# Kernel tuning notes

Measured on AMD Instinct MI355X. Metric: run time of the kernel, lower is better.

Reference implementation:

```python
import jax, jax.numpy as jnp
import numpy as np

B, N, L = 64, 256, 1024
OUT = L // 2   # ChebConv out_channels = Seq_len / 2
ALPHA = 0.5    # DirGNNConv default alpha


def _glorot(key, shape):
    # PyG ChebConv lins use glorot init
    lim = float(np.sqrt(6.0 / (shape[0] + shape[1])))
    return jax.random.uniform(key, shape, minval=-lim, maxval=lim, dtype=jnp.float32)


def setup_inputs() -> dict:
    key = jax.random.key(0)
    ks = jax.random.split(key, 8)
    x = jax.random.normal(ks[0], (B, N, L), dtype=jnp.float32)
    # dense per-sample adjacency; only used via nonzero() in torch, never enters math (K=1)
    At = jax.random.randint(ks[1], (B, N, N), 0, 2, dtype=jnp.int32)
    W_in = _glorot(ks[2], (L, OUT))
    b_in = jnp.zeros((OUT,), dtype=jnp.float32)
    W_out = _glorot(ks[3], (L, OUT))
    b_out = jnp.zeros((OUT,), dtype=jnp.float32)
    # DirGNNConv root Linear (kaiming-ish uniform; exact init irrelevant for correctness baseline)
    lim = float(1.0 / np.sqrt(L))
    W_root = jax.random.uniform(ks[4], (L, OUT), minval=-lim, maxval=lim, dtype=jnp.float32)
    b_root = jax.random.uniform(ks[5], (OUT,), minval=-lim, maxval=lim, dtype=jnp.float32)
    return {"x": x, "At": At, "W_in": W_in, "b_in": b_in,
            "W_out": W_out, "b_out": b_out, "W_root": W_root, "b_root": b_root}


def reference(x, At, W_in, b_in, W_out, b_out, W_root, b_root):
    # so the batched edge_index built from At.nonzero() never influences the output.
    # DirGNNConv: alpha * conv_out(x) + (1-alpha) * conv_in(x) + root_lin(x).
    xf = x.reshape(B * N, L)                        # [B*N, L]
    y = (ALPHA * (xf @ W_out + b_out)
         + (1.0 - ALPHA) * (xf @ W_in + b_in)
         + (xf @ W_root + b_root))                  # [B*N, OUT]
    return y.reshape(B, N, OUT)
```

## Files before the change

kernel.cpp:

```cpp
#include <hip/hip_runtime.h>
#include <stdint.h>

static constexpr int Mrows = 16384;
static constexpr int Kdim  = 1024;
static constexpr int Ncols = 512;

typedef __attribute__((ext_vector_type(8))) short bf16x8;
typedef __attribute__((ext_vector_type(4))) float f32x4;

__device__ __forceinline__ unsigned short f2bf(float f) {
  unsigned u = __builtin_bit_cast(unsigned, f);
  u += 0x7FFFu + ((u >> 16) & 1u);
  return (unsigned short)(u >> 16);
}
__device__ __forceinline__ unsigned f2bf2(float lo, float hi) {
  unsigned ul = __builtin_bit_cast(unsigned, lo);
  unsigned uh = __builtin_bit_cast(unsigned, hi);
  ul += 0x7FFFu + ((ul >> 16) & 1u);
  uh += 0x7FFFu + ((uh >> 16) & 1u);
  return (ul >> 16) | (uh & 0xFFFF0000u);
}

__global__ __launch_bounds__(256) void combine_w(
    const float* __restrict__ Win, const float* __restrict__ Wout,
    const float* __restrict__ Wroot, unsigned short* __restrict__ Wt)
{
  __shared__ unsigned short lds[32 * 36];
  const int bid = blockIdx.x;
  const int tk0 = (bid & 31) * 32;
  const int tn0 = (bid >> 5) * 32;
  const int t = threadIdx.x;
  {
    const int k  = t >> 3;
    const int nq = (t & 7) * 4;
    const int gi = (tk0 + k) * Ncols + tn0 + nq;
    const float4 wi = *(const float4*)(Win + gi);
    const float4 wo = *(const float4*)(Wout + gi);
    const float4 wr = *(const float4*)(Wroot + gi);
    lds[(nq + 0) * 36 + k] = f2bf(0.5f * (wi.x + wo.x) + wr.x);
    lds[(nq + 1) * 36 + k] = f2bf(0.5f * (wi.y + wo.y) + wr.y);
    lds[(nq + 2) * 36 + k] = f2bf(0.5f * (wi.z + wo.z) + wr.z);
    lds[(nq + 3) * 36 + k] = f2bf(0.5f * (wi.w + wo.w) + wr.w);
  }
  __syncthreads();
  {
    const int n  = t >> 3;
    const int k8 = (t & 7) * 4;
    const ushort4 v = *(const ushort4*)&lds[n * 36 + k8];
    *(ushort4*)(Wt + (size_t)(tn0 + n) * Kdim + tk0 + k8) = v;
  }
}

__global__ __launch_bounds__(256) void gemm_fused(
    const float* __restrict__ X, const unsigned short* __restrict__ Wt,
    const float* __restrict__ b_in, const float* __restrict__ b_out,
    const float* __restrict__ b_root, float* __restrict__ Y)
{
  __shared__ short Asl[128 * 40];
  __shared__ short Bsl[128 * 40];

  const int bid = blockIdx.x;
  const int m0 = (bid & 127) * 128;
  const int n0 = (bid >> 7) * 128;

  const int t    = threadIdx.x;
  const int lane = t & 63;
  const int wid  = t >> 6;
  const int wm   = wid >> 1;
  const int wn   = wid & 1;
  const int quad = lane >> 4;
  const int lm   = lane & 15;

  const int sr = t >> 1;
  const int sh = t & 1;
  const float*          xp = X  + (size_t)(m0 + sr) * Kdim + sh * 16;
  const unsigned short* wp = Wt + (size_t)(n0 + sr) * Kdim + sh * 16;
  const int sbase = sr * 40 + sh * 16;

  f32x4 acc[4][4] = {};

  float4 a0 = *(const float4*)(xp + 0);
  float4 a1 = *(const float4*)(xp + 4);
  float4 a2 = *(const float4*)(xp + 8);
  float4 a3 = *(const float4*)(xp + 12);
  uint4  bA = *(const uint4*)(wp);
  uint4  bB = *(const uint4*)(wp + 8);

  const int arow0 = (wm * 64 + lm) * 40 + quad * 8;
  const int brow0 = (wn * 64 + lm) * 40 + quad * 8;

  #pragma unroll 1
  for (int it = 0; it < 32; ++it) {
    __syncthreads();
    uint4 p0, p1;
    p0.x = f2bf2(a0.x, a0.y); p0.y = f2bf2(a0.z, a0.w);
    p0.z = f2bf2(a1.x, a1.y); p0.w = f2bf2(a1.z, a1.w);
    p1.x = f2bf2(a2.x, a2.y); p1.y = f2bf2(a2.z, a2.w);
    p1.z = f2bf2(a3.x, a3.y); p1.w = f2bf2(a3.z, a3.w);
    *(uint4*)&Asl[sbase]     = p0;
    *(uint4*)&Asl[sbase + 8] = p1;
    *(uint4*)&Bsl[sbase]     = bA;
    *(uint4*)&Bsl[sbase + 8] = bB;
    __syncthreads();

    if (it < 31) {
      const float* xn = xp + (it + 1) * 32;
      a0 = *(const float4*)(xn + 0);
      a1 = *(const float4*)(xn + 4);
      a2 = *(const float4*)(xn + 8);
      a3 = *(const float4*)(xn + 12);
      const unsigned short* wn2 = wp + (it + 1) * 32;
      bA = *(const uint4*)(wn2);
      bB = *(const uint4*)(wn2 + 8);
    }

    bf16x8 af[4], bfr[4];
    #pragma unroll
    for (int i = 0; i < 4; ++i) af[i]  = *(const bf16x8*)&Asl[arow0 + i * 16 * 40];
    #pragma unroll
    for (int j = 0; j < 4; ++j) bfr[j] = *(const bf16x8*)&Bsl[brow0 + j * 16 * 40];

    #pragma unroll
    for (int i = 0; i < 4; ++i)
      #pragma unroll
      for (int j = 0; j < 4; ++j)
        acc[i][j] = __builtin_amdgcn_mfma_f32_16x16x32_bf16(af[i], bfr[j], acc[i][j], 0, 0, 0);
  }

  #pragma unroll
  for (int j = 0; j < 4; ++j) {
    const int gc = n0 + wn * 64 + j * 16 + lm;
    const float bias = 0.5f * (b_in[gc] + b_out[gc]) + b_root[gc];
    #pragma unroll
    for (int i = 0; i < 4; ++i) {
      const int gr = m0 + wm * 64 + i * 16 + quad * 4;
      float* yp = Y + (size_t)gr * Ncols + gc;
      #pragma unroll
      for (int r = 0; r < 4; ++r)
        yp[(size_t)r * Ncols] = acc[i][j][r] + bias;
    }
  }
}

extern "C" void kernel_launch(void* const* d_in, const int* in_sizes, int n_in,
                              void* d_out, int out_size, void* d_ws, size_t ws_size,
                              hipStream_t stream)
{
  const float* x      = (const float*)d_in[0];
  const float* W_in   = (const float*)d_in[2];
  const float* b_in   = (const float*)d_in[3];
  const float* W_out  = (const float*)d_in[4];
  const float* b_out  = (const float*)d_in[5];
  const float* W_root = (const float*)d_in[6];
  const float* b_root = (const float*)d_in[7];
  float* y = (float*)d_out;

  unsigned short* Wt = (unsigned short*)d_ws;

  combine_w<<<dim3(512), dim3(256), 0, stream>>>(W_in, W_out, W_root, Wt);
  gemm_fused<<<dim3(512), dim3(256), 0, stream>>>(x, Wt, b_in, b_out, b_root, y);
}
```

Measured before the change: 155.7 us.

## Pre-convert X to bf16 and stage GEMM tiles via direct global-to-LDS loads

Adds a prep pass that converts X to bf16 into workspace, merged into one launch with the weight-combine blocks. The GEMM then streams bf16 tiles with global_load_lds into an XOR-swizzled unpadded LDS layout and drops the register prefetch and in-loop conversion. This cuts in-loop ALU work and register pressure, and launch bounds now request two blocks per SM. The cost is an extra full read and write of X through HBM, plus less overlap, since each iteration waits on its own loads before the MFMAs.

```diff
diff --git a/kernel.cpp b/kernel.cpp
--- a/kernel.cpp
+++ b/kernel.cpp
@@ -21,43 +21,62 @@
   return (ul >> 16) | (uh & 0xFFFF0000u);
 }
 
-__global__ __launch_bounds__(256) void combine_w(
+__device__ __forceinline__ void gl2lds16(const void* g, void* l) {
+  __builtin_amdgcn_global_load_lds(
+      (const __attribute__((address_space(1))) void*)g,
+      (__attribute__((address_space(3))) void*)l, 16, 0, 0);
+}
+
+__global__ __launch_bounds__(256) void prep(
+    const float* __restrict__ x,
     const float* __restrict__ Win, const float* __restrict__ Wout,
-    const float* __restrict__ Wroot, unsigned short* __restrict__ Wt)
+    const float* __restrict__ Wroot,
+    unsigned short* __restrict__ Xbf, unsigned short* __restrict__ Wt)
 {
-  __shared__ unsigned short lds[32 * 36];
   const int bid = blockIdx.x;
-  const int tk0 = (bid & 31) * 32;
-  const int tn0 = (bid >> 5) * 32;
   const int t = threadIdx.x;
-  {
-    const int k  = t >> 3;
-    const int nq = (t & 7) * 4;
-    const int gi = (tk0 + k) * Ncols + tn0 + nq;
-    const float4 wi = *(const float4*)(Win + gi);
-    const float4 wo = *(const float4*)(Wout + gi);
-    const float4 wr = *(const float4*)(Wroot + gi);
-    lds[(nq + 0) * 36 + k] = f2bf(0.5f * (wi.x + wo.x) + wr.x);
-    lds[(nq + 1) * 36 + k] = f2bf(0.5f * (wi.y + wo.y) + wr.y);
-    lds[(nq + 2) * 36 + k] = f2bf(0.5f * (wi.z + wo.z) + wr.z);
-    lds[(nq + 3) * 36 + k] = f2bf(0.5f * (wi.w + wo.w) + wr.w);
-  }
-  __syncthreads();
-  {
-    const int n  = t >> 3;
-    const int k8 = (t & 7) * 4;
-    const ushort4 v = *(const ushort4*)&lds[n * 36 + k8];
-    *(ushort4*)(Wt + (size_t)(tn0 + n) * Kdim + tk0 + k8) = v;
+  if (bid < 8192) {
+    const size_t base = ((size_t)bid * 256 + t) * 8;
+    const float4 v0 = *(const float4*)(x + base);
+    const float4 v1 = *(const float4*)(x + base + 4);
+    uint4 p;
+    p.x = f2bf2(v0.x, v0.y); p.y = f2bf2(v0.z, v0.w);
+    p.z = f2bf2(v1.x, v1.y); p.w = f2bf2(v1.z, v1.w);
+    *(uint4*)(Xbf + base) = p;
+  } else {
+    __shared__ unsigned short lds[32 * 36];
+    const int b2 = bid - 8192;
+    const int tk0 = (b2 & 31) * 32;
+    const int tn0 = (b2 >> 5) * 32;
+    {
+      const int k  = t >> 3;
+      const int nq = (t & 7) * 4;
+      const int gi = (tk0 + k) * Ncols + tn0 + nq;
+      const float4 wi = *(const float4*)(Win + gi);
+      const float4 wo = *(const float4*)(Wout + gi);
+      const float4 wr = *(const float4*)(Wroot + gi);
+      lds[(nq + 0) * 36 + k] = f2bf(0.5f * (wi.x + wo.x) + wr.x);
+      lds[(nq + 1) * 36 + k] = f2bf(0.5f * (wi.y + wo.y) + wr.y);
+      lds[(nq + 2) * 36 + k] = f2bf(0.5f * (wi.z + wo.z) + wr.z);
+      lds[(nq + 3) * 36 + k] = f2bf(0.5f * (wi.w + wo.w) + wr.w);
+    }
+    __syncthreads();
+    {
+      const int n  = t >> 3;
+      const int k8 = (t & 7) * 4;
+      const ushort4 v = *(const ushort4*)&lds[n * 36 + k8];
+      *(ushort4*)(Wt + (size_t)(tn0 + n) * Kdim + tk0 + k8) = v;
+    }
   }
 }
 
-__global__ __launch_bounds__(256) void gemm_fused(
-    const float* __restrict__ X, const unsigned short* __restrict__ Wt,
+__global__ __launch_bounds__(256, 2) void gemm_bf16(
+    const unsigned short* __restrict__ Xbf, const unsigned short* __restrict__ Wt,
     const float* __restrict__ b_in, const float* __restrict__ b_out,
     const float* __restrict__ b_root, float* __restrict__ Y)
 {
-  __shared__ short Asl[128 * 40];
-  __shared__ short Bsl[128 * 40];
+  __shared__ __attribute__((aligned(16))) short As[128 * 32];
+  __shared__ __attribute__((aligned(16))) short Bs[128 * 32];
 
   const int bid = blockIdx.x;
   const int m0 = (bid & 127) * 128;
@@ -65,66 +84,52 @@
 
   const int t    = threadIdx.x;
   const int lane = t & 63;
-  const int wid  = t >> 6;
-  const int wm   = wid >> 1;
-  const int wn   = wid & 1;
+  const int w    = t >> 6;
+  const int wm   = w >> 1;
+  const int wn   = w & 1;
   const int quad = lane >> 4;
   const int lm   = lane & 15;
 
-  const int sr = t >> 1;
-  const int sh = t & 1;
-  const float*          xp = X  + (size_t)(m0 + sr) * Kdim + sh * 16;
-  const unsigned short* wp = Wt + (size_t)(n0 + sr) * Kdim + sh * 16;
-  const int sbase = sr * 40 + sh * 16;
+  const int sr = lane >> 2;
+  const int ss = lane & 3;
+  const int sc = ss ^ ((sr >> 1) & 3);
+  const unsigned short* gA = Xbf + (size_t)(m0 + w * 32 + sr) * Kdim + sc * 8;
+  const unsigned short* gB = Wt  + (size_t)(n0 + w * 32 + sr) * Kdim + sc * 8;
+  short* const lA0 = &As[(w * 32) * 32];
+  short* const lA1 = &As[(w * 32 + 16) * 32];
+  short* const lB0 = &Bs[(w * 32) * 32];
+  short* const lB1 = &Bs[(w * 32 + 16) * 32];
+  const int rowK = 16 * Kdim;
+
+  const int slot = quad ^ ((lm >> 1) & 3);
+  const int aoff = (wm * 64 + lm) * 32 + slot * 8;
+  const int boff = (wn * 64 + lm) * 32 + slot * 8;
 
   f32x4 acc[4][4] = {};
 
-  float4 a0 = *(const float4*)(xp + 0);
-  float4 a1 = *(const float4*)(xp + 4);
-  float4 a2 = *(const float4*)(xp + 8);
-  float4 a3 = *(const float4*)(xp + 12);
-  uint4  bA = *(const uint4*)(wp);
-  uint4  bB = *(const uint4*)(wp + 8);
-
-  const int arow0 = (wm * 64 + lm) * 40 + quad * 8;
-  const int brow0 = (wn * 64 + lm) * 40 + quad * 8;
-
   #pragma unroll 1
   for (int it = 0; it < 32; ++it) {
+    const unsigned short* ga = gA + it * 32;
+    const unsigned short* gb = gB + it * 32;
+    gl2lds16(ga,        lA0);
+    gl2lds16(ga + rowK, lA1);
+    gl2lds16(gb,        lB0);
+    gl2lds16(gb + rowK, lB1);
     __syncthreads();
-    uint4 p0, p1;
-    p0.x = f2bf2(a0.x, a0.y); p0.y = f2bf2(a0.z, a0.w);
-    p0.z = f2bf2(a1.x, a1.y); p0.w = f2bf2(a1.z, a1.w);
-    p1.x = f2bf2(a2.x, a2.y); p1.y = f2bf2(a2.z, a2.w);
-    p1.z = f2bf2(a3.x, a3.y); p1.w = f2bf2(a3.z, a3.w);
-    *(uint4*)&Asl[sbase]     = p0;
-    *(uint4*)&Asl[sbase + 8] = p1;
-    *(uint4*)&Bsl[sbase]     = bA;
-    *(uint4*)&Bsl[sbase + 8] = bB;
-    __syncthreads();
-
-    if (it < 31) {
-      const float* xn = xp + (it + 1) * 32;
-      a0 = *(const float4*)(xn + 0);
-      a1 = *(const float4*)(xn + 4);
-      a2 = *(const float4*)(xn + 8);
-      a3 = *(const float4*)(xn + 12);
-      const unsigned short* wn2 = wp + (it + 1) * 32;
-      bA = *(const uint4*)(wn2);
-      bB = *(const uint4*)(wn2 + 8);
-    }
 
     bf16x8 af[4], bfr[4];
     #pragma unroll
-    for (int i = 0; i < 4; ++i) af[i]  = *(const bf16x8*)&Asl[arow0 + i * 16 * 40];
+    for (int i = 0; i < 4; ++i) af[i]  = *(const bf16x8*)&As[aoff + i * 16 * 32];
     #pragma unroll
-    for (int j = 0; j < 4; ++j) bfr[j] = *(const bf16x8*)&Bsl[brow0 + j * 16 * 40];
+    for (int j = 0; j < 4; ++j) bfr[j] = *(const bf16x8*)&Bs[boff + j * 16 * 32];
 
     #pragma unroll
     for (int i = 0; i < 4; ++i)
       #pragma unroll
       for (int j = 0; j < 4; ++j)
         acc[i][j] = __builtin_amdgcn_mfma_f32_16x16x32_bf16(af[i], bfr[j], acc[i][j], 0, 0, 0);
+
+    __syncthreads();
   }
 
   #pragma unroll
@@ -155,8 +160,9 @@
   const float* b_root = (const float*)d_in[7];
   float* y = (float*)d_out;
 
-  unsigned short* Wt = (unsigned short*)d_ws;
+  unsigned short* Xbf = (unsigned short*)d_ws;
+  unsigned short* Wt  = (unsigned short*)d_ws + (size_t)Mrows * Kdim;
 
-  combine_w<<<dim3(512), dim3(256), 0, stream>>>(W_in, W_out, W_root, Wt);
-  gemm_fused<<<dim3(512), dim3(256), 0, stream>>>(x, Wt, b_in, b_out, b_root, y);
+  prep<<<dim3(8192 + 512), dim3(256), 0, stream>>>(x, W_in, W_out, W_root, Xbf, Wt);
+  gemm_bf16<<<dim3(512), dim3(256), 0, stream>>>(Xbf, Wt, b_in, b_out, b_root, y);
 }
```

Result: no change. 155.0 us (-0.5%).

## Double-buffer LDS with direct global-to-LDS weight loads and XOR swizzle

Applied to the files above, without the earlier changes.

The GEMM now keeps two LDS buffers so it needs one barrier per K-step instead of two. Weight tiles are loaded straight into LDS with global_load_lds, and the bf16 conversion and store of the next X tile happen after the MFMAs so they overlap with compute. Padded rows are replaced by an XOR-swizzled layout to avoid bank conflicts, and launch bounds request two blocks per CU. The risks are extra LDS use, more register pressure, and a redundant final-iteration load.

```diff
diff --git a/kernel.cpp b/kernel.cpp
--- a/kernel.cpp
+++ b/kernel.cpp
@@ -1,7 +1,6 @@
 #include <hip/hip_runtime.h>
 #include <stdint.h>
 
-static constexpr int Mrows = 16384;
 static constexpr int Kdim  = 1024;
 static constexpr int Ncols = 512;
 
@@ -19,6 +18,12 @@
   ul += 0x7FFFu + ((ul >> 16) & 1u);
   uh += 0x7FFFu + ((uh >> 16) & 1u);
   return (ul >> 16) | (uh & 0xFFFF0000u);
+}
+
+__device__ __forceinline__ void gl2lds16(const void* g, void* l) {
+  __builtin_amdgcn_global_load_lds(
+      (const __attribute__((address_space(1))) void*)g,
+      (__attribute__((address_space(3))) void*)l, 16, 0, 0);
 }
 
 __global__ __launch_bounds__(256) void combine_w(
@@ -51,13 +56,13 @@
   }
 }
 
-__global__ __launch_bounds__(256) void gemm_fused(
+__global__ __launch_bounds__(256, 2) void gemm_fused2(
     const float* __restrict__ X, const unsigned short* __restrict__ Wt,
     const float* __restrict__ b_in, const float* __restrict__ b_out,
     const float* __restrict__ b_root, float* __restrict__ Y)
 {
-  __shared__ short Asl[128 * 40];
-  __shared__ short Bsl[128 * 40];
+  __shared__ __attribute__((aligned(16))) short As[2 * 4096];
+  __shared__ __attribute__((aligned(16))) short Bs[2 * 4096];
 
   const int bid = blockIdx.x;
   const int m0 = (bid & 127) * 128;
@@ -65,66 +70,81 @@
 
   const int t    = threadIdx.x;
   const int lane = t & 63;
-  const int wid  = t >> 6;
-  const int wm   = wid >> 1;
-  const int wn   = wid & 1;
+  const int w    = t >> 6;
+  const int wm   = w >> 1;
+  const int wn   = w & 1;
   const int quad = lane >> 4;
   const int lm   = lane & 15;
 
   const int sr = t >> 1;
   const int sh = t & 1;
-  const float*          xp = X  + (size_t)(m0 + sr) * Kdim + sh * 16;
-  const unsigned short* wp = Wt + (size_t)(n0 + sr) * Kdim + sh * 16;
-  const int sbase = sr * 40 + sh * 16;
+  const float* xp = X + (size_t)(m0 + sr) * Kdim + sh * 16;
+  const int sw  = (sr >> 1) & 3;
+  const int aw0 = sr * 32 + (((2 * sh) ^ sw) * 8);
+  const int aw1 = sr * 32 + (((2 * sh + 1) ^ sw) * 8);
+
+  const int srb = lane >> 2;
+  const int ss  = lane & 3;
+  const int sc  = ss ^ ((srb >> 1) & 3);
+  const unsigned short* gB = Wt + (size_t)(n0 + w * 32 + srb) * Kdim + sc * 8;
+  const int rowK = 16 * Kdim;
+  const int lb0 = w * 1024;
+  const int lb1 = w * 1024 + 512;
+
+  const int slot = quad ^ ((lm >> 1) & 3);
+  const int aoff = (wm * 64 + lm) * 32 + slot * 8;
+  const int boff = (wn * 64 + lm) * 32 + slot * 8;
 
   f32x4 acc[4][4] = {};
 
-  float4 a0 = *(const float4*)(xp + 0);
-  float4 a1 = *(const float4*)(xp + 4);
-  float4 a2 = *(const float4*)(xp + 8);
-  float4 a3 = *(const float4*)(xp + 12);
-  uint4  bA = *(const uint4*)(wp);
-  uint4  bB = *(const uint4*)(wp + 8);
-
-  const int arow0 = (wm * 64 + lm) * 40 + quad * 8;
-  const int brow0 = (wn * 64 + lm) * 40 + quad * 8;
-
-  #pragma unroll 1
-  for (int it = 0; it < 32; ++it) {
-    __syncthreads();
+  gl2lds16(gB,        &Bs[lb0]);
+  gl2lds16(gB + rowK, &Bs[lb1]);
+  {
+    const float4 a0 = *(const float4*)(xp + 0);
+    const float4 a1 = *(const float4*)(xp + 4);
+    const float4 a2 = *(const float4*)(xp + 8);
+    const float4 a3 = *(const float4*)(xp + 12);
     uint4 p0, p1;
     p0.x = f2bf2(a0.x, a0.y); p0.y = f2bf2(a0.z, a0.w);
     p0.z = f2bf2(a1.x, a1.y); p0.w = f2bf2(a1.z, a1.w);
     p1.x = f2bf2(a2.x, a2.y); p1.y = f2bf2(a2.z, a2.w);
     p1.z = f2bf2(a3.x, a3.y); p1.w = f2bf2(a3.z, a3.w);
-    *(uint4*)&Asl[sbase]     = p0;
-    *(uint4*)&Asl[sbase + 8] = p1;
-    *(uint4*)&Bsl[sbase]     = bA;
-    *(uint4*)&Bsl[sbase + 8] = bB;
+    *(uint4*)&As[aw0] = p0;
+    *(uint4*)&As[aw1] = p1;
+  }
+
+  #pragma unroll 1
+  for (int it = 0; it < 32; ++it) {
+    const int p = (it & 1) * 4096;
+    const int q = p ^ 4096;
     __syncthreads();
 
-    if (it < 31) {
-      const float* xn = xp + (it + 1) * 32;
-      a0 = *(const float4*)(xn + 0);
-      a1 = *(const float4*)(xn + 4);
-      a2 = *(const float4*)(xn + 8);
-      a3 = *(const float4*)(xn + 12);
-      const unsigned short* wn2 = wp + (it + 1) * 32;
-      bA = *(const uint4*)(wn2);
-      bB = *(const uint4*)(wn2 + 8);
-    }
+    const int nx = (it < 31 ? it + 1 : 31) * 32;
+    gl2lds16(gB + nx,        &Bs[q + lb0]);
+    gl2lds16(gB + nx + rowK, &Bs[q + lb1]);
+    const float4 a0 = *(const float4*)(xp + nx + 0);
+    const float4 a1 = *(const float4*)(xp + nx + 4);
+    const float4 a2 = *(const float4*)(xp + nx + 8);
+    const float4 a3 = *(const float4*)(xp + nx + 12);
 
     bf16x8 af[4], bfr[4];
     #pragma unroll
-    for (int i = 0; i < 4; ++i) af[i]  = *(const bf16x8*)&Asl[arow0 + i * 16 * 40];
+    for (int i = 0; i < 4; ++i) af[i]  = *(const bf16x8*)&As[p + aoff + i * 512];
     #pragma unroll
-    for (int j = 0; j < 4; ++j) bfr[j] = *(const bf16x8*)&Bsl[brow0 + j * 16 * 40];
-
+    for (int j = 0; j < 4; ++j) bfr[j] = *(const bf16x8*)&Bs[p + boff + j * 512];
     #pragma unroll
     for (int i = 0; i < 4; ++i)
       #pragma unroll
       for (int j = 0; j < 4; ++j)
         acc[i][j] = __builtin_amdgcn_mfma_f32_16x16x32_bf16(af[i], bfr[j], acc[i][j], 0, 0, 0);
+
+    uint4 p0, p1;
+    p0.x = f2bf2(a0.x, a0.y); p0.y = f2bf2(a0.z, a0.w);
+    p0.z = f2bf2(a1.x, a1.y); p0.w = f2bf2(a1.z, a1.w);
+    p1.x = f2bf2(a2.x, a2.y); p1.y = f2bf2(a2.z, a2.w);
+    p1.z = f2bf2(a3.x, a3.y); p1.w = f2bf2(a3.z, a3.w);
+    *(uint4*)&As[q + aw0] = p0;
+    *(uint4*)&As[q + aw1] = p1;
   }
 
   #pragma unroll
@@ -157,6 +177,6 @@
 
   unsigned short* Wt = (unsigned short*)d_ws;
 
-  combine_w<<<dim3(512), dim3(256), 0, stream>>>(W_in, W_out, W_root, Wt);
-  gemm_fused<<<dim3(512), dim3(256), 0, stream>>>(x, Wt, b_in, b_out, b_root, y);
+  combine_w <<<dim3(512), dim3(256), 0, stream>>>(W_in, W_out, W_root, Wt);
+  gemm_fused2<<<dim3(512), dim3(256), 0, stream>>>(x, Wt, b_in, b_out, b_root, y);
 }
```

After: 161.4 us. +3.6%, slower.
